# Optimization experiments

Hardware: AMD Instinct MI355X
Metric: run time of the kernel (lower is better)

Reference implementation:

```python
import jax, jax.numpy as jnp
import numpy as np

N = 50000
D = 128           # feature_dim
H = 8             # num_heads
DH = D // H       # head_dim = 16
K = 32            # k_neighbors
FFN = int(D * 1.5)  # 192
TAU_NEG = 0.6
BETA = 1.5
LN_EPS = 1e-5


def layer_norm(x, g, b):
    mu = jnp.mean(x, axis=-1, keepdims=True)
    var = jnp.mean((x - mu) ** 2, axis=-1, keepdims=True)
    return (x - mu) * jax.lax.rsqrt(var + LN_EPS) * g + b


def setup_inputs() -> dict:
    key = jax.random.key(0)
    ks = jax.random.split(key, 12)
    s = 1.0 / np.sqrt(D)
    inp = {
        "features": jax.random.normal(ks[0], (N, D), dtype=jnp.float32),
        "knn_indices": jax.random.randint(ks[1], (N, K), 0, N, dtype=jnp.int64 if jax.config.jax_enable_x64 else jnp.int32),
        "spatial_distances": jax.random.uniform(ks[2], (N, K), dtype=jnp.float32) * 8.0,
        "Wq": jax.random.normal(ks[3], (D, D), dtype=jnp.float32) * s,
        "Wk": jax.random.normal(ks[4], (D, D), dtype=jnp.float32) * s,
        "Wv": jax.random.normal(ks[5], (D, D), dtype=jnp.float32) * s,
        "Wo": jax.random.normal(ks[6], (D, D), dtype=jnp.float32) * s,
        "bo": jnp.zeros((D,), dtype=jnp.float32),
        "ln1_g": jnp.ones((D,), dtype=jnp.float32),
        "ln1_b": jnp.zeros((D,), dtype=jnp.float32),
        "W1": jax.random.normal(ks[7], (D, FFN), dtype=jnp.float32) * s,
        "b1": jnp.zeros((FFN,), dtype=jnp.float32),
        "W2": jax.random.normal(ks[8], (FFN, D), dtype=jnp.float32) * (1.0 / np.sqrt(FFN)),
        "b2": jnp.zeros((D,), dtype=jnp.float32),
        "ln2_g": jnp.ones((D,), dtype=jnp.float32),
        "ln2_b": jnp.zeros((D,), dtype=jnp.float32),
    }
    return inp


def reference(features, knn_indices, spatial_distances, Wq, Wk, Wv, Wo, bo,
              ln1_g, ln1_b, W1, b1, W2, b2, ln2_g, ln2_b):
    n = features.shape[0]
    Q = (features @ Wq).reshape(n, H, DH)           # (N,H,dh)
    Kp = (features @ Wk).reshape(n, H, DH)
    Vp = (features @ Wv).reshape(n, H, DH)

    K_local = Kp[knn_indices]                        # (N,K,H,dh) irregular gather
    V_local = Vp[knn_indices]                        # (N,K,H,dh)

    raw_scores = jnp.einsum("nhd,nkhd->nhk", Q, K_local) / np.sqrt(DH)  # (N,H,K)

    # per-head spatial decay: 1 / 2^(h+1)
    head_scalings = (0.5 ** jnp.arange(1, H + 1, dtype=features.dtype))  # (H,)
    scaled_dist = spatial_distances[:, None, :] * head_scalings[None, :, None]  # (N,H,K)

    attn_pos = jax.nn.softmax(raw_scores - scaled_dist, axis=-1)
    attn_neg = jax.nn.softmax((-raw_scores - scaled_dist) / TAU_NEG, axis=-1)
    attn = attn_pos - BETA * attn_neg                # (N,H,K); dropout is identity in eval

    attended = jnp.einsum("nhk,nkhd->nhd", attn, V_local).reshape(n, D)

    x = attended @ Wo + bo + features
    x = layer_norm(x, ln1_g, ln1_b)

    h = jax.nn.gelu(x @ W1 + b1, approximate=False)
    ffn_out = h @ W2 + b2
    out = layer_norm(ffn_out + x, ln2_g, ln2_b)
    return out
```

## Files before the change

kernel.cpp:

```cpp
#include <hip/hip_runtime.h>
#include <hip/hip_fp16.h>
#include <cmath>

typedef __attribute__((ext_vector_type(8))) _Float16 f16x8;
typedef __attribute__((ext_vector_type(4))) float f32x4;

__device__ __forceinline__ unsigned int pkh(float a, float b) {
    __half2 h = __floats2half2_rn(a, b);
    return *(unsigned int*)&h;
}
__device__ __forceinline__ float gelu_exact(float v) {
    return 0.5f * v * (1.0f + erff(v * 0.70710678118654752440f));
}
__device__ __forceinline__ __half2 shfl8h(__half2 x, int m) {
    int xi = *(int*)&x;
    int yi = __shfl_xor(xi, m, 8);
    return *(__half2*)&yi;
}

__global__ __launch_bounds__(256, 1) void k_prep(
    const float* __restrict__ Wq, const float* __restrict__ Wk, const float* __restrict__ Wv,
    const float* __restrict__ Wo, const float* __restrict__ W1, const float* __restrict__ W2,
    unsigned short* __restrict__ wsz)
{
    int f = blockIdx.x * 256 + threadIdx.x;
    const float* W; unsigned short* dst; int M, KS, fl;
    if (f < 2048)       { W = Wq; dst = wsz;         M = 128; KS = 4; fl = f; }
    else if (f < 4096)  { W = Wk; dst = wsz + 16384; M = 128; KS = 4; fl = f - 2048; }
    else if (f < 6144)  { W = Wv; dst = wsz + 32768; M = 128; KS = 4; fl = f - 4096; }
    else if (f < 8192)  { W = Wo; dst = wsz + 49152; M = 128; KS = 4; fl = f - 6144; }
    else if (f < 11264) { W = W1; dst = wsz + 65536; M = 192; KS = 4; fl = f - 8192; }
    else if (f < 14336) { W = W2; dst = wsz + 90112; M = 128; KS = 6; fl = f - 11264; }
    else return;
    const int l  = fl & 63;
    const int ks = (fl >> 6) % KS;
    const int ct = (fl >> 6) / KS;
    const int k0 = ks * 32 + (l >> 4) * 8;
    const int col = ct * 16 + (l & 15);
    unsigned short tmp[8];
    #pragma unroll
    for (int j = 0; j < 8; ++j) {
        __half hh = __float2half(W[(size_t)(k0 + j) * M + col]);
        tmp[j] = *(unsigned short*)&hh;
    }
    ((uint4*)dst)[fl] = *(uint4*)tmp;
}

__global__ __launch_bounds__(256, 4) void k_qkv(
    const float* __restrict__ feat, const unsigned short* __restrict__ wsz,
    unsigned short* __restrict__ Qb, unsigned short* __restrict__ KVb, int n)
{
    const int w = threadIdx.x >> 6, lane = threadIdx.x & 63;
    const int lrow = lane & 15, kgrp = lane >> 4;
    const int node = blockIdx.x * 64 + w * 16 + lrow;
    const bool valid = node < n;

    f16x8 bfr[4];
    #pragma unroll
    for (int ks = 0; ks < 4; ++ks) {
        float4 lo = make_float4(0.f, 0.f, 0.f, 0.f), hi = lo;
        if (valid) {
            const float* p = feat + (size_t)node * 128 + ks * 32 + kgrp * 8;
            lo = *(const float4*)p;
            hi = *(const float4*)(p + 4);
        }
        f16x8 b;
        b[0] = (_Float16)lo.x; b[1] = (_Float16)lo.y; b[2] = (_Float16)lo.z; b[3] = (_Float16)lo.w;
        b[4] = (_Float16)hi.x; b[5] = (_Float16)hi.y; b[6] = (_Float16)hi.z; b[7] = (_Float16)hi.w;
        bfr[ks] = b;
    }

    for (int mat = 0; mat < 3; ++mat) {
        const unsigned short* wb = wsz + mat * 16384;
        f32x4 acc[8];
        #pragma unroll
        for (int ct = 0; ct < 8; ++ct) acc[ct] = (f32x4){0.f, 0.f, 0.f, 0.f};
        #pragma unroll
        for (int ct = 0; ct < 8; ++ct)
            #pragma unroll
            for (int ks = 0; ks < 4; ++ks) {
                f16x8 afr = *(const f16x8*)(wb + ((size_t)(ct * 4 + ks) * 64 + lane) * 8);
                acc[ct] = __builtin_amdgcn_mfma_f32_16x16x32_f16(afr, bfr[ks], acc[ct], 0, 0, 0);
            }
        if (valid) {
            unsigned short* O = (mat == 0) ? (Qb + (size_t)node * 128)
                              : (KVb + (size_t)node * 256 + (mat == 2 ? 128 : 0));
            #pragma unroll
            for (int ct = 0; ct < 8; ++ct) {
                int col = ct * 16 + kgrp * 4;
                *((uint2*)(O + col)) =
                    make_uint2(pkh(acc[ct][0], acc[ct][1]), pkh(acc[ct][2], acc[ct][3]));
            }
        }
    }
}

__global__ __launch_bounds__(256, 4) void k_attn(
    const unsigned short* __restrict__ Qb, const unsigned short* __restrict__ KVb,
    const int* __restrict__ knn, const float* __restrict__ dist,
    unsigned short* __restrict__ attf, int n)
{
    const int lane = threadIdx.x & 63;
    const int node = blockIdx.x * 4 + (threadIdx.x >> 6);
    if (node >= n) return;
    const int h = lane >> 3, r = lane & 7;
    const float hs = exp2f(-(float)(h + 1));

    int idx[4]; float sd[4];
    #pragma unroll
    for (int jj = 0; jj < 4; ++jj) {
        int j = r + jj * 8;
        idx[jj] = knn[(size_t)node * 32 + j];
        sd[jj]  = dist[(size_t)node * 32 + j] * hs;
    }

    const unsigned short* qp = Qb + (size_t)node * 128 + h * 16;
    __half2 q2[8];
    *((uint4*)&q2[0]) = *(const uint4*)qp;
    *((uint4*)&q2[4]) = *(const uint4*)(qp + 8);

    uint4 k0[4], k1[4], v0[4], v1[4];
    #pragma unroll
    for (int jj = 0; jj < 4; ++jj) {
        const unsigned short* kvp = KVb + (size_t)idx[jj] * 256 + h * 16;
        k0[jj] = *(const uint4*)kvp;
        k1[jj] = *(const uint4*)(kvp + 8);
        v0[jj] = *(const uint4*)(kvp + 128);
        v1[jj] = *(const uint4*)(kvp + 136);
    }

    float ap[4], an[4];
    #pragma unroll
    for (int jj = 0; jj < 4; ++jj) {
        const __half2* ka = (const __half2*)&k0[jj];
        const __half2* kb = (const __half2*)&k1[jj];
        __half2 s0 = __hmul2(q2[0], ka[0]);
        s0 = __hfma2(q2[1], ka[1], s0);
        s0 = __hfma2(q2[2], ka[2], s0);
        s0 = __hfma2(q2[3], ka[3], s0);
        __half2 s1 = __hmul2(q2[4], kb[0]);
        s1 = __hfma2(q2[5], kb[1], s1);
        s1 = __hfma2(q2[6], kb[2], s1);
        s1 = __hfma2(q2[7], kb[3], s1);
        float s = __low2float(s0) + __high2float(s0) + __low2float(s1) + __high2float(s1);
        float raw = s * 0.25f;
        ap[jj] = raw - sd[jj];
        an[jj] = (-raw - sd[jj]) * (1.0f / 0.6f);
    }

    float mp = fmaxf(fmaxf(ap[0], ap[1]), fmaxf(ap[2], ap[3]));
    float mn = fmaxf(fmaxf(an[0], an[1]), fmaxf(an[2], an[3]));
    #pragma unroll
    for (int msk = 1; msk < 8; msk <<= 1) {
        mp = fmaxf(mp, __shfl_xor(mp, msk, 8));
        mn = fmaxf(mn, __shfl_xor(mn, msk, 8));
    }
    float ep[4], en[4], sp = 0.f, sn = 0.f;
    #pragma unroll
    for (int jj = 0; jj < 4; ++jj) {
        ep[jj] = expf(ap[jj] - mp); sp += ep[jj];
        en[jj] = expf(an[jj] - mn); sn += en[jj];
    }
    #pragma unroll
    for (int msk = 1; msk < 8; msk <<= 1) {
        sp += __shfl_xor(sp, msk, 8);
        sn += __shfl_xor(sn, msk, 8);
    }
    const float isp = 1.0f / sp;
    const float isn = 1.5f / sn;

    __half2 acc2[8];
    #pragma unroll
    for (int i = 0; i < 8; ++i) acc2[i] = __float2half2_rn(0.f);
    #pragma unroll
    for (int jj = 0; jj < 4; ++jj) {
        float wgt = ep[jj] * isp - en[jj] * isn;
        __half2 w2 = __float2half2_rn(wgt);
        const __half2* va = (const __half2*)&v0[jj];
        const __half2* vb = (const __half2*)&v1[jj];
        acc2[0] = __hfma2(w2, va[0], acc2[0]);
        acc2[1] = __hfma2(w2, va[1], acc2[1]);
        acc2[2] = __hfma2(w2, va[2], acc2[2]);
        acc2[3] = __hfma2(w2, va[3], acc2[3]);
        acc2[4] = __hfma2(w2, vb[0], acc2[4]);
        acc2[5] = __hfma2(w2, vb[1], acc2[5]);
        acc2[6] = __hfma2(w2, vb[2], acc2[6]);
        acc2[7] = __hfma2(w2, vb[3], acc2[7]);
    }
    #pragma unroll
    for (int i = 0; i < 8; ++i) {
        acc2[i] = __hadd2(acc2[i], shfl8h(acc2[i], 1));
        acc2[i] = __hadd2(acc2[i], shfl8h(acc2[i], 2));
        acc2[i] = __hadd2(acc2[i], shfl8h(acc2[i], 4));
    }
    if (r == 0) {
        const int g = node >> 4, lrow = node & 15;
        unsigned short* op = attf + (size_t)g * 2048 + (h >> 1) * 512 + (h & 1) * 256 + lrow * 8;
        *((uint4*)op)         = *(uint4*)&acc2[0];
        *((uint4*)(op + 128)) = *(uint4*)&acc2[4];
    }
}

__global__ __launch_bounds__(256, 4) void k_tail(
    const unsigned short* __restrict__ attf, const float* __restrict__ feat,
    const unsigned short* __restrict__ wsz,
    const float* __restrict__ bo, const float* __restrict__ g1, const float* __restrict__ b1ln,
    const float* __restrict__ b1f, const float* __restrict__ b2f,
    const float* __restrict__ g2, const float* __restrict__ b2ln,
    float* __restrict__ out, int n)
{
    __shared__ __align__(16) unsigned short hls[12288];
    const int tid = threadIdx.x;
    const int w = tid >> 6, lane = tid & 63;
    const int lrow = lane & 15, kgrp = lane >> 4;
    const int node = blockIdx.x * 64 + w * 16 + lrow;
    const bool valid = node < n;
    const int g = blockIdx.x * 4 + w;

    f16x8 bfr[6];
    #pragma unroll
    for (int ks = 0; ks < 4; ++ks) {
        uint4 u = make_uint4(0u, 0u, 0u, 0u);
        if (valid) u = *(const uint4*)(attf + (size_t)g * 2048 + ks * 512 + kgrp * 128 + lrow * 8);
        bfr[ks] = *(f16x8*)&u;
    }
    const unsigned short* wo = wsz + 49152;
    f32x4 X[8];
    #pragma unroll
    for (int ct = 0; ct < 8; ++ct) {
        X[ct] = (f32x4){0.f, 0.f, 0.f, 0.f};
        #pragma unroll
        for (int ks = 0; ks < 4; ++ks) {
            f16x8 afr = *(const f16x8*)(wo + ((size_t)(ct * 4 + ks) * 64 + lane) * 8);
            X[ct] = __builtin_amdgcn_mfma_f32_16x16x32_f16(afr, bfr[ks], X[ct], 0, 0, 0);
        }
    }
    #pragma unroll
    for (int ct = 0; ct < 8; ++ct) {
        int col = ct * 16 + kgrp * 4;
        float4 bv = *((const float4*)(bo + col));
        float4 fr = make_float4(0.f, 0.f, 0.f, 0.f);
        if (valid) fr = *((const float4*)(feat + (size_t)node * 128 + col));
        X[ct][0] += bv.x + fr.x; X[ct][1] += bv.y + fr.y;
        X[ct][2] += bv.z + fr.z; X[ct][3] += bv.w + fr.w;
    }
    float s = 0.f;
    #pragma unroll
    for (int ct = 0; ct < 8; ++ct) s += X[ct][0] + X[ct][1] + X[ct][2] + X[ct][3];
    s += __shfl_xor(s, 16); s += __shfl_xor(s, 32);
    const float mu1 = s * (1.0f / 128.0f);
    float s2 = 0.f;
    #pragma unroll
    for (int ct = 0; ct < 8; ++ct)
        #pragma unroll
        for (int rr = 0; rr < 4; ++rr) { float d = X[ct][rr] - mu1; s2 = fmaf(d, d, s2); }
    s2 += __shfl_xor(s2, 16); s2 += __shfl_xor(s2, 32);
    const float rs1 = rsqrtf(s2 * (1.0f / 128.0f) + 1e-5f);

    uint2 xnh[8];
    #pragma unroll
    for (int ct = 0; ct < 8; ++ct) {
        int col = ct * 16 + kgrp * 4;
        float4 gg = *((const float4*)(g1 + col));
        float4 bb = *((const float4*)(b1ln + col));
        float x0 = (X[ct][0] - mu1) * rs1 * gg.x + bb.x;
        float x1 = (X[ct][1] - mu1) * rs1 * gg.y + bb.y;
        float x2 = (X[ct][2] - mu1) * rs1 * gg.z + bb.z;
        float x3 = (X[ct][3] - mu1) * rs1 * gg.w + bb.w;
        xnh[ct] = make_uint2(pkh(x0, x1), pkh(x2, x3));
        int ks = col >> 5, kg = (col & 31) >> 3, jb = col & 7;
        *((uint2*)&hls[((w * 4 + ks) * 4 + kg) * 128 + lrow * 8 + jb]) = xnh[ct];
    }
    __syncthreads();
    #pragma unroll
    for (int ks = 0; ks < 4; ++ks)
        bfr[ks] = *(const f16x8*)&hls[((w * 4 + ks) * 4 + kgrp) * 128 + lrow * 8];
    __syncthreads();

    const unsigned short* w1 = wsz + 65536;
    #pragma unroll
    for (int ct = 0; ct < 12; ++ct) {
        f32x4 acc = (f32x4){0.f, 0.f, 0.f, 0.f};
        #pragma unroll
        for (int ks = 0; ks < 4; ++ks) {
            f16x8 afr = *(const f16x8*)(w1 + ((size_t)(ct * 4 + ks) * 64 + lane) * 8);
            acc = __builtin_amdgcn_mfma_f32_16x16x32_f16(afr, bfr[ks], acc, 0, 0, 0);
        }
        int col = ct * 16 + kgrp * 4;
        float4 bv = *((const float4*)(b1f + col));
        float h0 = gelu_exact(acc[0] + bv.x);
        float h1 = gelu_exact(acc[1] + bv.y);
        float h2 = gelu_exact(acc[2] + bv.z);
        float h3 = gelu_exact(acc[3] + bv.w);
        int ks = col >> 5, kg = (col & 31) >> 3, jb = col & 7;
        *((uint2*)&hls[((w * 6 + ks) * 4 + kg) * 128 + lrow * 8 + jb]) =
            make_uint2(pkh(h0, h1), pkh(h2, h3));
    }
    __syncthreads();
    #pragma unroll
    for (int ks = 0; ks < 6; ++ks)
        bfr[ks] = *(const f16x8*)&hls[((w * 6 + ks) * 4 + kgrp) * 128 + lrow * 8];

    const unsigned short* w2 = wsz + 90112;
    f32x4 Y[8];
    #pragma unroll
    for (int ct = 0; ct < 8; ++ct) {
        Y[ct] = (f32x4){0.f, 0.f, 0.f, 0.f};
        #pragma unroll
        for (int ks = 0; ks < 6; ++ks) {
            f16x8 afr = *(const f16x8*)(w2 + ((size_t)(ct * 6 + ks) * 64 + lane) * 8);
            Y[ct] = __builtin_amdgcn_mfma_f32_16x16x32_f16(afr, bfr[ks], Y[ct], 0, 0, 0);
        }
    }
    #pragma unroll
    for (int ct = 0; ct < 8; ++ct) {
        int col = ct * 16 + kgrp * 4;
        float4 bv = *((const float4*)(b2f + col));
        __half2 x01 = *(__half2*)&xnh[ct].x, x23 = *(__half2*)&xnh[ct].y;
        Y[ct][0] += bv.x + __low2float(x01);
        Y[ct][1] += bv.y + __high2float(x01);
        Y[ct][2] += bv.z + __low2float(x23);
        Y[ct][3] += bv.w + __high2float(x23);
    }
    float t1 = 0.f;
    #pragma unroll
    for (int ct = 0; ct < 8; ++ct) t1 += Y[ct][0] + Y[ct][1] + Y[ct][2] + Y[ct][3];
    t1 += __shfl_xor(t1, 16); t1 += __shfl_xor(t1, 32);
    const float mu2 = t1 * (1.0f / 128.0f);
    float t2 = 0.f;
    #pragma unroll
    for (int ct = 0; ct < 8; ++ct)
        #pragma unroll
        for (int rr = 0; rr < 4; ++rr) { float d = Y[ct][rr] - mu2; t2 = fmaf(d, d, t2); }
    t2 += __shfl_xor(t2, 16); t2 += __shfl_xor(t2, 32);
    const float rs2 = rsqrtf(t2 * (1.0f / 128.0f) + 1e-5f);
    if (valid) {
        #pragma unroll
        for (int ct = 0; ct < 8; ++ct) {
            int col = ct * 16 + kgrp * 4;
            float4 gg = *((const float4*)(g2 + col));
            float4 bb = *((const float4*)(b2ln + col));
            float4 o;
            o.x = (Y[ct][0] - mu2) * rs2 * gg.x + bb.x;
            o.y = (Y[ct][1] - mu2) * rs2 * gg.y + bb.y;
            o.z = (Y[ct][2] - mu2) * rs2 * gg.z + bb.z;
            o.w = (Y[ct][3] - mu2) * rs2 * gg.w + bb.w;
            *((float4*)(out + (size_t)node * 128 + col)) = o;
        }
    }
}

extern "C" void kernel_launch(void* const* d_in, const int* in_sizes, int n_in,
                              void* d_out, int out_size, void* d_ws, size_t ws_size,
                              hipStream_t stream)
{
    const float* feat = (const float*)d_in[0];
    const int*   knn  = (const int*)d_in[1];
    const float* dist = (const float*)d_in[2];
    const float* Wq   = (const float*)d_in[3];
    const float* Wk   = (const float*)d_in[4];
    const float* Wv   = (const float*)d_in[5];
    const float* Wo   = (const float*)d_in[6];
    const float* bo   = (const float*)d_in[7];
    const float* g1   = (const float*)d_in[8];
    const float* b1ln = (const float*)d_in[9];
    const float* W1   = (const float*)d_in[10];
    const float* b1f  = (const float*)d_in[11];
    const float* W2   = (const float*)d_in[12];
    const float* b2f  = (const float*)d_in[13];
    const float* g2   = (const float*)d_in[14];
    const float* b2ln = (const float*)d_in[15];
    float* out = (float*)d_out;

    const int n = in_sizes[0] / 128;
    const size_t ND = (size_t)n * 128;
    if (ws_size < 8 * ND + 262144) return;

    unsigned short* Qb   = (unsigned short*)d_ws;
    unsigned short* KVb  = Qb + ND;
    unsigned short* attf = KVb + 2 * ND;
    unsigned short* Wsz  = attf + ND;

    k_prep<<<56, 256, 0, stream>>>(Wq, Wk, Wv, Wo, W1, W2, Wsz);
    k_qkv <<<(n + 63) / 64, 256, 0, stream>>>(feat, Wsz, Qb, KVb, n);
    k_attn<<<(n + 3) / 4,   256, 0, stream>>>(Qb, KVb, knn, dist, attf, n);
    k_tail<<<(n + 63) / 64, 256, 0, stream>>>(attf, feat, Wsz, bo, g1, b1ln, b1f, b2f,
                                              g2, b2ln, out, n);
}
```

Before: 179.8 us.

## Apply grab-bag of micro-optimizations: fast GELU, exp2 softmax, nontemporal IO, prep split

Replaces exact erf GELU with a sigmoid-based polynomial approximation, and folds log2(e) into the softmax inputs so exp2f can replace expf. Adds nontemporal loads and stores in the attention and tail kernels, and hoists the residual feature loads ahead of the Wo MFMA loop. Splits the weight-prep work across twice as many threads and raises k_qkv occupancy to 8 waves. The GELU approximation changes numerics slightly and may affect accuracy tolerance.

Result: slower. 184.5 us (+2.6%).

```diff
diff --git a/kernel.cpp b/kernel.cpp
--- a/kernel.cpp
+++ b/kernel.cpp
@@ -4,13 +4,15 @@
 
 typedef __attribute__((ext_vector_type(8))) _Float16 f16x8;
 typedef __attribute__((ext_vector_type(4))) float f32x4;
+typedef __attribute__((ext_vector_type(4))) unsigned int u32x4;
 
 __device__ __forceinline__ unsigned int pkh(float a, float b) {
     __half2 h = __floats2half2_rn(a, b);
     return *(unsigned int*)&h;
 }
-__device__ __forceinline__ float gelu_exact(float v) {
-    return 0.5f * v * (1.0f + erff(v * 0.70710678118654752440f));
+__device__ __forceinline__ float gelu_fast(float x) {
+    float w = x * fmaf(x * x, 0.1029377202f, 2.302085565f);
+    return x * __builtin_amdgcn_rcpf(1.0f + exp2f(-w));
 }
 __device__ __forceinline__ __half2 shfl8h(__half2 x, int m) {
     int xi = *(int*)&x;
@@ -23,30 +25,32 @@
     const float* __restrict__ Wo, const float* __restrict__ W1, const float* __restrict__ W2,
     unsigned short* __restrict__ wsz)
 {
-    int f = blockIdx.x * 256 + threadIdx.x;
+    int idx = blockIdx.x * 256 + threadIdx.x;
+    if (idx >= 28672) return;
+    int f = idx >> 1;
+    const int half = idx & 1;
     const float* W; unsigned short* dst; int M, KS, fl;
     if (f < 2048)       { W = Wq; dst = wsz;         M = 128; KS = 4; fl = f; }
     else if (f < 4096)  { W = Wk; dst = wsz + 16384; M = 128; KS = 4; fl = f - 2048; }
     else if (f < 6144)  { W = Wv; dst = wsz + 32768; M = 128; KS = 4; fl = f - 4096; }
     else if (f < 8192)  { W = Wo; dst = wsz + 49152; M = 128; KS = 4; fl = f - 6144; }
     else if (f < 11264) { W = W1; dst = wsz + 65536; M = 192; KS = 4; fl = f - 8192; }
-    else if (f < 14336) { W = W2; dst = wsz + 90112; M = 128; KS = 6; fl = f - 11264; }
-    else return;
+    else                { W = W2; dst = wsz + 90112; M = 128; KS = 6; fl = f - 11264; }
     const int l  = fl & 63;
     const int ks = (fl >> 6) % KS;
     const int ct = (fl >> 6) / KS;
-    const int k0 = ks * 32 + (l >> 4) * 8;
+    const int k0 = ks * 32 + (l >> 4) * 8 + half * 4;
     const int col = ct * 16 + (l & 15);
-    unsigned short tmp[8];
-    #pragma unroll
-    for (int j = 0; j < 8; ++j) {
+    unsigned short tmp[4];
+    #pragma unroll
+    for (int j = 0; j < 4; ++j) {
         __half hh = __float2half(W[(size_t)(k0 + j) * M + col]);
         tmp[j] = *(unsigned short*)&hh;
     }
-    ((uint4*)dst)[fl] = *(uint4*)tmp;
-}
-
-__global__ __launch_bounds__(256, 4) void k_qkv(
+    ((uint2*)dst)[fl * 2 + half] = *(uint2*)tmp;
+}
+
+__global__ __launch_bounds__(256, 8) void k_qkv(
     const float* __restrict__ feat, const unsigned short* __restrict__ wsz,
     unsigned short* __restrict__ Qb, unsigned short* __restrict__ KVb, int n)
 {
@@ -104,20 +108,21 @@
     const int node = blockIdx.x * 4 + (threadIdx.x >> 6);
     if (node >= n) return;
     const int h = lane >> 3, r = lane & 7;
-    const float hs = exp2f(-(float)(h + 1));
-
-    int idx[4]; float sd[4];
+    const float L2E = 1.4426950408889634f;
+    const float hsl = exp2f(-(float)(h + 1)) * L2E;
+
+    int idx[4]; float sdl[4];
     #pragma unroll
     for (int jj = 0; jj < 4; ++jj) {
         int j = r + jj * 8;
-        idx[jj] = knn[(size_t)node * 32 + j];
-        sd[jj]  = dist[(size_t)node * 32 + j] * hs;
+        idx[jj] = __builtin_nontemporal_load(knn + (size_t)node * 32 + j);
+        sdl[jj] = __builtin_nontemporal_load(dist + (size_t)node * 32 + j) * hsl;
     }
 
     const unsigned short* qp = Qb + (size_t)node * 128 + h * 16;
     __half2 q2[8];
-    *((uint4*)&q2[0]) = *(const uint4*)qp;
-    *((uint4*)&q2[4]) = *(const uint4*)(qp + 8);
+    *((u32x4*)&q2[0]) = __builtin_nontemporal_load((const u32x4*)qp);
+    *((u32x4*)&q2[4]) = __builtin_nontemporal_load((const u32x4*)(qp + 8));
 
     uint4 k0[4], k1[4], v0[4], v1[4];
     #pragma unroll
@@ -143,9 +148,9 @@
         s1 = __hfma2(q2[6], kb[2], s1);
         s1 = __hfma2(q2[7], kb[3], s1);
         float s = __low2float(s0) + __high2float(s0) + __low2float(s1) + __high2float(s1);
-        float raw = s * 0.25f;
-        ap[jj] = raw - sd[jj];
-        an[jj] = (-raw - sd[jj]) * (1.0f / 0.6f);
+        float rawl = s * (0.25f * L2E);
+        ap[jj] = rawl - sdl[jj];
+        an[jj] = (-rawl - sdl[jj]) * (1.0f / 0.6f);
     }
 
     float mp = fmaxf(fmaxf(ap[0], ap[1]), fmaxf(ap[2], ap[3]));
@@ -158,8 +163,8 @@
     float ep[4], en[4], sp = 0.f, sn = 0.f;
     #pragma unroll
     for (int jj = 0; jj < 4; ++jj) {
-        ep[jj] = expf(ap[jj] - mp); sp += ep[jj];
-        en[jj] = expf(an[jj] - mn); sn += en[jj];
+        ep[jj] = exp2f(ap[jj] - mp); sp += ep[jj];
+        en[jj] = exp2f(an[jj] - mn); sn += en[jj];
     }
     #pragma unroll
     for (int msk = 1; msk < 8; msk <<= 1) {
@@ -196,8 +201,8 @@
     if (r == 0) {
         const int g = node >> 4, lrow = node & 15;
         unsigned short* op = attf + (size_t)g * 2048 + (h >> 1) * 512 + (h & 1) * 256 + lrow * 8;
-        *((uint4*)op)         = *(uint4*)&acc2[0];
-        *((uint4*)(op + 128)) = *(uint4*)&acc2[4];
+        __builtin_nontemporal_store(*(u32x4*)&acc2[0], (u32x4*)op);
+        __builtin_nontemporal_store(*(u32x4*)&acc2[4], (u32x4*)(op + 128));
     }
 }
 
@@ -221,9 +226,16 @@
     #pragma unroll
     for (int ks = 0; ks < 4; ++ks) {
         uint4 u = make_uint4(0u, 0u, 0u, 0u);
-        if (valid) u = *(const uint4*)(attf + (size_t)g * 2048 + ks * 512 + kgrp * 128 + lrow * 8);
+        if (valid) u = *(const uint4*)(attf + (size_t)g * 2048 + (ks * 4 + kgrp) * 128 + lrow * 8);
         bfr[ks] = *(f16x8*)&u;
     }
+    float4 fr[8];
+    #pragma unroll
+    for (int ct = 0; ct < 8; ++ct) {
+        fr[ct] = make_float4(0.f, 0.f, 0.f, 0.f);
+        if (valid) fr[ct] = *((const float4*)(feat + (size_t)node * 128 + ct * 16 + kgrp * 4));
+    }
+
     const unsigned short* wo = wsz + 49152;
     f32x4 X[8];
     #pragma unroll
@@ -239,10 +251,8 @@
     for (int ct = 0; ct < 8; ++ct) {
         int col = ct * 16 + kgrp * 4;
         float4 bv = *((const float4*)(bo + col));
-        float4 fr = make_float4(0.f, 0.f, 0.f, 0.f);
-        if (valid) fr = *((const float4*)(feat + (size_t)node * 128 + col));
-        X[ct][0] += bv.x + fr.x; X[ct][1] += bv.y + fr.y;
-        X[ct][2] += bv.z + fr.z; X[ct][3] += bv.w + fr.w;
+        X[ct][0] += bv.x + fr[ct].x; X[ct][1] += bv.y + fr[ct].y;
+        X[ct][2] += bv.z + fr[ct].z; X[ct][3] += bv.w + fr[ct].w;
     }
     float s = 0.f;
     #pragma unroll
@@ -268,13 +278,13 @@
         float x2 = (X[ct][2] - mu1) * rs1 * gg.z + bb.z;
         float x3 = (X[ct][3] - mu1) * rs1 * gg.w + bb.w;
         xnh[ct] = make_uint2(pkh(x0, x1), pkh(x2, x3));
-        int ks = col >> 5, kg = (col & 31) >> 3, jb = col & 7;
-        *((uint2*)&hls[((w * 4 + ks) * 4 + kg) * 128 + lrow * 8 + jb]) = xnh[ct];
+        int ks4 = col >> 5, kg = (col & 31) >> 3, jb = col & 7;
+        *((uint2*)&hls[w * 2048 + (ks4 * 4 + kg) * 128 + lrow * 8 + jb]) = xnh[ct];
     }
     __syncthreads();
     #pragma unroll
     for (int ks = 0; ks < 4; ++ks)
-        bfr[ks] = *(const f16x8*)&hls[((w * 4 + ks) * 4 + kgrp) * 128 + lrow * 8];
+        bfr[ks] = *(const f16x8*)&hls[w * 2048 + (ks * 4 + kgrp) * 128 + lrow * 8];
     __syncthreads();
 
     const unsigned short* w1 = wsz + 65536;
@@ -288,18 +298,17 @@
         }
         int col = ct * 16 + kgrp * 4;
         float4 bv = *((const float4*)(b1f + col));
-        float h0 = gelu_exact(acc[0] + bv.x);
-        float h1 = gelu_exact(acc[1] + bv.y);
-        float h2 = gelu_exact(acc[2] + bv.z);
-        float h3 = gelu_exact(acc[3] + bv.w);
-        int ks = col >> 5, kg = (col & 31) >> 3, jb = col & 7;
-        *((uint2*)&hls[((w * 6 + ks) * 4 + kg) * 128 + lrow * 8 + jb]) =
+        float h0 = gelu_fast(acc[0] + bv.x), h1 = gelu_fast(acc[1] + bv.y);
+        float h2 = gelu_fast(acc[2] + bv.z), h3 = gelu_fast(acc[3] + bv.w);
+        int ks6 = col >> 5, kg = (col & 31) >> 3, jb = col & 7;
+        *((uint2*)&hls[w * 3072 + (ks6 * 4 + kg) * 128 + lrow * 8 + jb]) =
             make_uint2(pkh(h0, h1), pkh(h2, h3));
     }
     __syncthreads();
+    f16x8 bfh[6];
     #pragma unroll
     for (int ks = 0; ks < 6; ++ks)
-        bfr[ks] = *(const f16x8*)&hls[((w * 6 + ks) * 4 + kgrp) * 128 + lrow * 8];
+        bfh[ks] = *(const f16x8*)&hls[w * 3072 + (ks * 4 + kgrp) * 128 + lrow * 8];
 
     const unsigned short* w2 = wsz + 90112;
     f32x4 Y[8];
@@ -309,7 +318,7 @@
         #pragma unroll
         for (int ks = 0; ks < 6; ++ks) {
             f16x8 afr = *(const f16x8*)(w2 + ((size_t)(ct * 6 + ks) * 64 + lane) * 8);
-            Y[ct] = __builtin_amdgcn_mfma_f32_16x16x32_f16(afr, bfr[ks], Y[ct], 0, 0, 0);
+            Y[ct] = __builtin_amdgcn_mfma_f32_16x16x32_f16(afr, bfh[ks], Y[ct], 0, 0, 0);
         }
     }
     #pragma unroll
@@ -340,12 +349,12 @@
             int col = ct * 16 + kgrp * 4;
             float4 gg = *((const float4*)(g2 + col));
             float4 bb = *((const float4*)(b2ln + col));
-            float4 o;
-            o.x = (Y[ct][0] - mu2) * rs2 * gg.x + bb.x;
-            o.y = (Y[ct][1] - mu2) * rs2 * gg.y + bb.y;
-            o.z = (Y[ct][2] - mu2) * rs2 * gg.z + bb.z;
-            o.w = (Y[ct][3] - mu2) * rs2 * gg.w + bb.w;
-            *((float4*)(out + (size_t)node * 128 + col)) = o;
+            f32x4 o;
+            o[0] = (Y[ct][0] - mu2) * rs2 * gg.x + bb.x;
+            o[1] = (Y[ct][1] - mu2) * rs2 * gg.y + bb.y;
+            o[2] = (Y[ct][2] - mu2) * rs2 * gg.z + bb.z;
+            o[3] = (Y[ct][3] - mu2) * rs2 * gg.w + bb.w;
+            __builtin_nontemporal_store(o, (f32x4*)(out + (size_t)node * 128 + col));
         }
     }
 }
@@ -381,7 +390,7 @@
     unsigned short* attf = KVb + 2 * ND;
     unsigned short* Wsz  = attf + ND;
 
-    k_prep<<<56, 256, 0, stream>>>(Wq, Wk, Wv, Wo, W1, W2, Wsz);
+    k_prep<<<112, 256, 0, stream>>>(Wq, Wk, Wv, Wo, W1, W2, Wsz);
     k_qkv <<<(n + 63) / 64, 256, 0, stream>>>(feat, Wsz, Qb, KVb, n);
     k_attn<<<(n + 3) / 4,   256, 0, stream>>>(Qb, KVb, knn, dist, attf, n);
     k_tail<<<(n + 63) / 64, 256, 0, stream>>>(attf, feat, Wsz, bo, g1, b1ln, b1f, b2f,
```
